# Performance work log

Hardware: AMD Instinct MI355X
Metric: run time of the kernel (lower is better)

Reference implementation:

```python
import jax, jax.numpy as jnp
import numpy as np

BIG_NUMBER = 1000000.0
B, N, F, D = 8, 256, 128, 128  # batch, nodes, feat dim, mid/out size


def setup_inputs() -> dict:
    key = jax.random.key(0)
    ks = jax.random.split(key, 16)
    node_fts = jax.random.normal(ks[0], (B, N, F), jnp.float32)
    hidden = jax.random.normal(ks[1], (B, N, F), jnp.float32)
    edge_fts = jax.random.normal(ks[2], (B, N, N, F), jnp.float32)
    e_hidden = jax.random.normal(ks[3], (B, N, N, F), jnp.float32)
    graph_fts = jax.random.normal(ks[4], (B, F), jnp.float32)
    adj_mat = jax.random.randint(ks[5], (B, N, N), 0, 2, jnp.int32)
    s = 0.05
    We = jax.random.normal(ks[6], (2 * F, D), jnp.float32) * s
    be = jnp.zeros((D,), jnp.float32)
    W_m1 = jax.random.normal(ks[7], (2 * F, D), jnp.float32) * s
    b_m1 = jnp.zeros((D,), jnp.float32)
    W_m2 = jax.random.normal(ks[8], (2 * F, D), jnp.float32) * s
    b_m2 = jnp.zeros((D,), jnp.float32)
    W_o1 = jax.random.normal(ks[9], (2 * F, D), jnp.float32) * s
    b_o1 = jnp.zeros((D,), jnp.float32)
    W_o2 = jax.random.normal(ks[10], (D, D), jnp.float32) * s
    b_o2 = jnp.zeros((D,), jnp.float32)
    return dict(node_fts=node_fts, edge_fts=edge_fts, graph_fts=graph_fts,
                adj_mat=adj_mat, hidden=hidden, e_hidden=e_hidden,
                We=We, be=be, W_m1=W_m1, b_m1=b_m1, W_m2=W_m2, b_m2=b_m2,
                W_o1=W_o1, b_o1=b_o1, W_o2=W_o2, b_o2=b_o2)


def reference(node_fts, edge_fts, graph_fts, adj_mat, hidden, e_hidden,
              We, be, W_m1, b_m1, W_m2, b_m2, W_o1, b_o1, W_o2, b_o2):
    # concat node/edge feats with hiddens
    nt = jnp.concatenate([node_fts, hidden], axis=-1)            # [B,N,2F]
    et = jnp.concatenate([edge_fts, e_hidden], axis=-1) @ We + be  # [B,N,N,D]
    # append virtual node (zeros features, fully connected)
    nt = jnp.concatenate([nt, jnp.zeros((B, 1, 2 * F), nt.dtype)], axis=1)  # [B,N+1,2F]
    adj = adj_mat.astype(nt.dtype)
    adj = jnp.concatenate([adj, jnp.ones((B, 1, N), nt.dtype)], axis=1)
    adj = jnp.concatenate([adj, jnp.ones((B, N + 1, 1), nt.dtype)], axis=2)  # [B,N+1,N+1]
    # MPNN layer (reduction = max)
    msg_1 = nt @ W_m1 + b_m1  # [B,N+1,D]
    msg_2 = nt @ W_m2 + b_m2  # [B,N+1,D]
    msgs = msg_1[:, None, :, :] + msg_2[:, :, None, :]  # [B,N+1,N+1,D]
    msgs = jnp.where(adj[..., None] > 0, msgs, -BIG_NUMBER)
    msgs = jnp.max(msgs, axis=1)  # [B,N+1,D]
    ret = (nt @ W_o1 + b_o1) + (msgs @ W_o2 + b_o2)  # [B,N+1,D]
    # strip virtual node; padded edge tensor sliced back equals et
    return ret[:, :N, :], et
```

## Files before the change

kernel.cpp:

```cpp
#include <hip/hip_runtime.h>
#include <hip/hip_bf16.h>

#define Bn 8
#define Nn 256
#define Fn 128
#define Dn 128

typedef __bf16 bf16_t;
typedef bf16_t bf16x8 __attribute__((ext_vector_type(8)));
typedef float f32x4 __attribute__((ext_vector_type(4)));

__global__ __launch_bounds__(256, 2) void mfma_gemm_kernel(
    const float* __restrict__ X1, const float* __restrict__ X2,
    const float* __restrict__ W, const float* __restrict__ bias,
    float* __restrict__ out)
{
    __shared__ __align__(16) bf16_t lds[128 * 256];

    const int t = threadIdx.x;

    for (int i = 0; i < 16; ++i) {
        int h  = t + i * 256;
        int k  = h >> 4;
        int n0 = (h & 15) * 8;
        f32x4 v0 = *(const f32x4*)(W + k * 128 + n0);
        f32x4 v1 = *(const f32x4*)(W + k * 128 + n0 + 4);
        int cc = k >> 3, kj = k & 7;
        float vv[8] = {v0[0], v0[1], v0[2], v0[3], v1[0], v1[1], v1[2], v1[3]};
        #pragma unroll
        for (int j = 0; j < 8; ++j) {
            int n  = n0 + j;
            int cp = cc ^ (n & 7);
            lds[n * 256 + cp * 8 + kj] = (bf16_t)vv[j];
        }
    }
    __syncthreads();

    const int wv = t >> 6;
    const int l  = t & 63;
    const int lane16 = l & 15;
    const int quad   = l >> 4;

    float bev[8];
    #pragma unroll
    for (int nt = 0; nt < 8; ++nt) bev[nt] = bias[nt * 16 + lane16];

    const long wrow = ((long)blockIdx.x * 4 + wv) * 64;

    for (int it = 0; it < 4; ++it) {
        const long rbase = wrow + it * 16;
        const long arow  = rbase + lane16;
        const float* pe = X1 + arow * 128 + quad * 8;
        const float* ph = X2 + arow * 128 + quad * 8;

        bf16x8 a[8];
        #pragma unroll
        for (int kk = 0; kk < 4; ++kk) {
            f32x4 u0 = *(const f32x4*)(pe + kk * 32);
            f32x4 u1 = *(const f32x4*)(pe + kk * 32 + 4);
            bf16x8 aa;
            #pragma unroll
            for (int j = 0; j < 4; ++j) { aa[j] = (bf16_t)u0[j]; aa[j + 4] = (bf16_t)u1[j]; }
            a[kk] = aa;
        }
        #pragma unroll
        for (int kk = 0; kk < 4; ++kk) {
            f32x4 u0 = *(const f32x4*)(ph + kk * 32);
            f32x4 u1 = *(const f32x4*)(ph + kk * 32 + 4);
            bf16x8 aa;
            #pragma unroll
            for (int j = 0; j < 4; ++j) { aa[j] = (bf16_t)u0[j]; aa[j + 4] = (bf16_t)u1[j]; }
            a[kk + 4] = aa;
        }

        f32x4 acc[8];
        #pragma unroll
        for (int nt = 0; nt < 8; ++nt) acc[nt] = (f32x4){0.f, 0.f, 0.f, 0.f};

        #pragma unroll
        for (int kk = 0; kk < 8; ++kk) {
            #pragma unroll
            for (int nt = 0; nt < 8; ++nt) {
                int n = nt * 16 + lane16;
                int c = kk * 4 + quad;
                bf16x8 bfrag = *(const bf16x8*)(&lds[n * 256 + (c ^ (n & 7)) * 8]);
                acc[nt] = __builtin_amdgcn_mfma_f32_16x16x32_bf16(a[kk], bfrag, acc[nt], 0, 0, 0);
            }
        }

        const long orow0 = rbase + quad * 4;
        #pragma unroll
        for (int nt = 0; nt < 8; ++nt) {
            #pragma unroll
            for (int r = 0; r < 4; ++r) {
                out[(orow0 + r) * 128 + nt * 16 + lane16] = acc[nt][r] + bev[nt];
            }
        }
    }
}

__global__ void ret_kernel(
    const int* __restrict__ adj,
    const float* __restrict__ m2, const float* __restrict__ m1,
    const float* __restrict__ h1,
    const float* __restrict__ W_o2, const float* __restrict__ b_o2,
    const float* __restrict__ b_m2,
    float* __restrict__ out)
{
    __shared__ float sv[128];
    __shared__ int adjc[256];

    const int bj = blockIdx.x;
    const int b  = bj >> 8;
    const int j  = bj & 255;
    const int d  = threadIdx.x;

    adjc[d]       = adj[(b * 256 + d) * 256 + j];
    adjc[d + 128] = adj[(b * 256 + d + 128) * 256 + j];
    __syncthreads();

    float mx = b_m2[d];
    const float* m2b = m2 + (long)b * 256 * 128 + d;
    for (int i = 0; i < 256; ++i) {
        if (adjc[i] != 0) {
            mx = fmaxf(mx, m2b[i * 128]);
        }
    }

    sv[d] = m1[bj * 128 + d] + mx;
    __syncthreads();

    float r = h1[bj * 128 + d] + b_o2[d];
    #pragma unroll 8
    for (int k = 0; k < 128; ++k)
        r += sv[k] * W_o2[k * 128 + d];

    out[bj * 128 + d] = r;
}

extern "C" void kernel_launch(void* const* d_in, const int* in_sizes, int n_in,
                              void* d_out, int out_size, void* d_ws, size_t ws_size,
                              hipStream_t stream)
{
    const float* node   = (const float*)d_in[0];
    const float* edge   = (const float*)d_in[1];
    const int*   adj    = (const int*)d_in[3];
    const float* hidden = (const float*)d_in[4];
    const float* ehid   = (const float*)d_in[5];
    const float* We     = (const float*)d_in[6];
    const float* be     = (const float*)d_in[7];
    const float* W_m1   = (const float*)d_in[8];
    const float* b_m1   = (const float*)d_in[9];
    const float* W_m2   = (const float*)d_in[10];
    const float* b_m2   = (const float*)d_in[11];
    const float* W_o1   = (const float*)d_in[12];
    const float* b_o1   = (const float*)d_in[13];
    const float* W_o2   = (const float*)d_in[14];
    const float* b_o2   = (const float*)d_in[15];

    float* out_ret = (float*)d_out;
    float* out_et  = (float*)d_out + Bn * Nn * Dn;

    float* ws_m2 = (float*)d_ws;
    float* ws_m1 = ws_m2 + 2048 * 128;
    float* ws_h1 = ws_m1 + 2048 * 128;

    hipLaunchKernelGGL(mfma_gemm_kernel, dim3(2048), dim3(256), 0, stream,
                       edge, ehid, We, be, out_et);
    hipLaunchKernelGGL(mfma_gemm_kernel, dim3(8), dim3(256), 0, stream,
                       node, hidden, W_m2, b_m2, ws_m2);
    hipLaunchKernelGGL(mfma_gemm_kernel, dim3(8), dim3(256), 0, stream,
                       node, hidden, W_m1, b_m1, ws_m1);
    hipLaunchKernelGGL(mfma_gemm_kernel, dim3(8), dim3(256), 0, stream,
                       node, hidden, W_o1, b_o1, ws_h1);
    hipLaunchKernelGGL(ret_kernel, dim3(2048), dim3(128), 0, stream,
                       adj, ws_m2, ws_m1, ws_h1, W_o2, b_o2, b_m2, out_ret);
}
```

Before: 745.8 us.

## Merge GEMM launches into one 512-thread kernel with vectorized swizzled LDS staging

Fuses the edge GEMM and the three small node GEMMs into a single launch, using 512-thread blocks that each cover 256 rows. This doubles the waves per block so more memory traffic is in flight per CU. The weight tile is now staged into LDS with 16-byte bf16x8 stores under a new two-level XOR swizzle, instead of scalar bf16 stores. The masked max loop in ret_kernel becomes a branchless select with unrolling. The trade-offs are heavier register pressure under the new launch bounds and per-block branching to pick which GEMM to run.

```diff
diff --git a/kernel.cpp b/kernel.cpp
--- a/kernel.cpp
+++ b/kernel.cpp
@@ -10,34 +10,62 @@
 typedef bf16_t bf16x8 __attribute__((ext_vector_type(8)));
 typedef float f32x4 __attribute__((ext_vector_type(4)));
 
-__global__ __launch_bounds__(256, 2) void mfma_gemm_kernel(
-    const float* __restrict__ X1, const float* __restrict__ X2,
-    const float* __restrict__ W, const float* __restrict__ bias,
-    float* __restrict__ out)
+__global__ __launch_bounds__(512, 4) void mfma_gemm_kernel(
+    const float* __restrict__ edge, const float* __restrict__ ehid,
+    const float* __restrict__ We,   const float* __restrict__ be,
+    const float* __restrict__ node, const float* __restrict__ hidden,
+    const float* __restrict__ W_m1, const float* __restrict__ b_m1,
+    const float* __restrict__ W_m2, const float* __restrict__ b_m2,
+    const float* __restrict__ W_o1, const float* __restrict__ b_o1,
+    float* __restrict__ out_et,
+    float* __restrict__ ws_m1, float* __restrict__ ws_m2, float* __restrict__ ws_h1)
 {
     __shared__ __align__(16) bf16_t lds[128 * 256];
 
     const int t = threadIdx.x;
 
-    for (int i = 0; i < 16; ++i) {
-        int h  = t + i * 256;
-        int k  = h >> 4;
-        int n0 = (h & 15) * 8;
-        f32x4 v0 = *(const f32x4*)(W + k * 128 + n0);
-        f32x4 v1 = *(const f32x4*)(W + k * 128 + n0 + 4);
-        int cc = k >> 3, kj = k & 7;
-        float vv[8] = {v0[0], v0[1], v0[2], v0[3], v1[0], v1[1], v1[2], v1[3]};
+    const float *X1, *X2, *W, *bias;
+    float* out;
+    long rowbase;
+    if (blockIdx.x < 2048) {
+        X1 = edge; X2 = ehid; W = We; bias = be; out = out_et;
+        rowbase = (long)blockIdx.x * 256;
+    } else {
+        const int e = blockIdx.x - 2048;
+        const int w = e >> 3;
+        rowbase = (long)(e & 7) * 256;
+        X1 = node; X2 = hidden;
+        if (w == 0)      { W = W_m2; bias = b_m2; out = ws_m2; }
+        else if (w == 1) { W = W_m1; bias = b_m1; out = ws_m1; }
+        else             { W = W_o1; bias = b_o1; out = ws_h1; }
+    }
+
+    {
+        const int kb = t >> 4;
+        const int g  = t & 15;
+        const float* wp = W + (kb * 8) * 128 + g * 8;
+        float buf[8][8];
+        #pragma unroll
+        for (int r = 0; r < 8; ++r) {
+            f32x4 u0 = *(const f32x4*)(wp + r * 128);
+            f32x4 u1 = *(const f32x4*)(wp + r * 128 + 4);
+            buf[r][0] = u0[0]; buf[r][1] = u0[1]; buf[r][2] = u0[2]; buf[r][3] = u0[3];
+            buf[r][4] = u1[0]; buf[r][5] = u1[1]; buf[r][6] = u1[2]; buf[r][7] = u1[3];
+        }
         #pragma unroll
         for (int j = 0; j < 8; ++j) {
-            int n  = n0 + j;
-            int cp = cc ^ (n & 7);
-            lds[n * 256 + cp * 8 + kj] = (bf16_t)vv[j];
+            const int n  = g * 8 + j;
+            const int cp = kb ^ j ^ (g & 7);
+            bf16x8 w8;
+            #pragma unroll
+            for (int r = 0; r < 8; ++r) w8[r] = (bf16_t)buf[r][j];
+            *(bf16x8*)(&lds[n * 256 + cp * 8]) = w8;
         }
     }
     __syncthreads();
 
-    const int wv = t >> 6;
-    const int l  = t & 63;
+    const int wv     = t >> 6;
+    const int l      = t & 63;
     const int lane16 = l & 15;
     const int quad   = l >> 4;
 
@@ -45,9 +73,9 @@
     #pragma unroll
     for (int nt = 0; nt < 8; ++nt) bev[nt] = bias[nt * 16 + lane16];
 
-    const long wrow = ((long)blockIdx.x * 4 + wv) * 64;
-
-    for (int it = 0; it < 4; ++it) {
+    const long wrow = rowbase + wv * 32;
+
+    for (int it = 0; it < 2; ++it) {
         const long rbase = wrow + it * 16;
         const long arow  = rbase + lane16;
         const float* pe = X1 + arow * 128 + quad * 8;
@@ -81,9 +109,10 @@
         for (int kk = 0; kk < 8; ++kk) {
             #pragma unroll
             for (int nt = 0; nt < 8; ++nt) {
-                int n = nt * 16 + lane16;
-                int c = kk * 4 + quad;
-                bf16x8 bfrag = *(const bf16x8*)(&lds[n * 256 + (c ^ (n & 7)) * 8]);
+                const int n  = nt * 16 + lane16;
+                const int c  = kk * 4 + quad;
+                const int cp = c ^ (n & 7) ^ ((n >> 3) & 7);
+                bf16x8 bfrag = *(const bf16x8*)(&lds[n * 256 + cp * 8]);
                 acc[nt] = __builtin_amdgcn_mfma_f32_16x16x32_bf16(a[kk], bfrag, acc[nt], 0, 0, 0);
             }
         }
@@ -121,10 +150,10 @@
 
     float mx = b_m2[d];
     const float* m2b = m2 + (long)b * 256 * 128 + d;
+    #pragma unroll 4
     for (int i = 0; i < 256; ++i) {
-        if (adjc[i] != 0) {
-            mx = fmaxf(mx, m2b[i * 128]);
-        }
+        const float v = adjc[i] ? m2b[i * 128] : -3.0e38f;
+        mx = fmaxf(mx, v);
     }
 
     sv[d] = m1[bj * 128 + d] + mx;
@@ -165,14 +194,10 @@
     float* ws_m1 = ws_m2 + 2048 * 128;
     float* ws_h1 = ws_m1 + 2048 * 128;
 
-    hipLaunchKernelGGL(mfma_gemm_kernel, dim3(2048), dim3(256), 0, stream,
-                       edge, ehid, We, be, out_et);
-    hipLaunchKernelGGL(mfma_gemm_kernel, dim3(8), dim3(256), 0, stream,
-                       node, hidden, W_m2, b_m2, ws_m2);
-    hipLaunchKernelGGL(mfma_gemm_kernel, dim3(8), dim3(256), 0, stream,
-                       node, hidden, W_m1, b_m1, ws_m1);
-    hipLaunchKernelGGL(mfma_gemm_kernel, dim3(8), dim3(256), 0, stream,
-                       node, hidden, W_o1, b_o1, ws_h1);
+    hipLaunchKernelGGL(mfma_gemm_kernel, dim3(2048 + 24), dim3(512), 0, stream,
+                       edge, ehid, We, be, node, hidden,
+                       W_m1, b_m1, W_m2, b_m2, W_o1, b_o1,
+                       out_et, ws_m1, ws_m2, ws_h1);
     hipLaunchKernelGGL(ret_kernel, dim3(2048), dim3(128), 0, stream,
                        adj, ws_m2, ws_m1, ws_h1, W_o2, b_o2, b_m2, out_ret);
 }
```

Result: faster. 679.8 us (-8.8%).
